# Performance work log

Measured on AMD Instinct MI355X. Metric: run time of the kernel, lower is better.

The kernel has to match this reference:

```python
import jax, jax.numpy as jnp
import numpy as np

B, C, S, D = 16, 32, 64, 512
DFF, E = 2048, 8


def setup_inputs() -> dict:
    key = jax.random.key(0)
    ks = jax.random.split(key, 16)
    std = 0.02
    return {
        'x': jax.random.normal(ks[0], (B, C, S, D), jnp.float32),
        'baseline': jax.random.normal(ks[1], (B, C, S, D), jnp.float32),
        'attnres': jax.random.normal(ks[2], (B, C, S, D), jnp.float32),
        'shared_w1': jax.random.normal(ks[3], (DFF, D), jnp.float32) * std,
        'shared_b1': jnp.zeros((DFF,), jnp.float32),
        'shared_w2': jax.random.normal(ks[4], (D, DFF), jnp.float32) * std,
        'shared_b2': jnp.zeros((D,), jnp.float32),
        'spa_router_w': jax.random.normal(ks[5], (E, 3 * D), jnp.float32) * std,
        'spa_router_b': jnp.zeros((E,), jnp.float32),
        'spe_router_w': jax.random.normal(ks[6], (E, 3 * D), jnp.float32) * std,
        'spe_router_b': jnp.zeros((E,), jnp.float32),
        'spa_w1': jax.random.normal(ks[7], (E, DFF, D), jnp.float32) * std,
        'spa_b1': jnp.zeros((E, DFF), jnp.float32),
        'spa_w2': jax.random.normal(ks[8], (E, D, DFF), jnp.float32) * std,
        'spa_b2': jnp.zeros((E, D), jnp.float32),
        'spe_w1': jax.random.normal(ks[9], (E, DFF, D), jnp.float32) * std,
        'spe_b1': jnp.zeros((E, DFF), jnp.float32),
        'spe_w2': jax.random.normal(ks[10], (E, D, DFF), jnp.float32) * std,
        'spe_b2': jnp.zeros((E, D), jnp.float32),
    }


def _route(feat, rw, rb):
    # feat [B, 3D] -> top-1 expert index [B] and its softmax gate weight [B]
    logits = feat @ rw.T + rb            # [B, E]
    p = jax.nn.softmax(logits, axis=-1)
    idx = jnp.argmax(logits, axis=-1)    # [B]
    w = jnp.take_along_axis(p, idx[:, None], axis=-1)[:, 0]
    return idx, w


def _specialist(xf, idx, w1, b1, w2, b2):
    # xf [B, T, D]; per-sample gather of expert weights then batched FFN
    W1, B1 = w1[idx], b1[idx]            # [B, DFF, D], [B, DFF]
    W2, B2 = w2[idx], b2[idx]            # [B, D, DFF], [B, D]
    h = jax.nn.gelu(jnp.einsum('btd,bfd->btf', xf, W1) + B1[:, None, :])
    return jnp.einsum('btf,bdf->btd', h, W2) + B2[:, None, :]


def reference(x, baseline, attnres, shared_w1, shared_b1, shared_w2, shared_b2,
              spa_router_w, spa_router_b, spe_router_w, spe_router_b,
              spa_w1, spa_b1, spa_w2, spa_b2, spe_w1, spe_b1, spe_w2, spe_b2):
    b, d = x.shape[0], x.shape[-1]
    xf = x.reshape(b, -1, d)  # [B, T, D]
    # sample-level AttnRes router features: [B, 3*d_model]
    feat = jnp.concatenate([
        baseline.mean(axis=(1, 2)),
        attnres.mean(axis=(1, 2)),
        (attnres - baseline).mean(axis=(1, 2)),
    ], axis=-1)
    spa_idx, spa_w = _route(feat, spa_router_w, spa_router_b)
    spe_idx, spe_w = _route(feat, spe_router_w, spe_router_b)
    # shared dense FFN (dropout=0 eval)
    shared = jax.nn.gelu(xf @ shared_w1.T + shared_b1) @ shared_w2.T + shared_b2
    spa_out = _specialist(xf, spa_idx, spa_w1, spa_b1, spa_w2, spa_b2)
    spe_out = _specialist(xf, spe_idx, spe_w1, spe_b1, spe_w2, spe_b2)
    y = shared + spa_w[:, None, None] * spa_out + spe_w[:, None, None] * spe_out
    return y.reshape(x.shape)
```

## Files before the change

kernel.cpp:

```cpp
#include <hip/hip_runtime.h>
#include <cstdint>
#include <cstddef>

#define DEV __device__ __forceinline__

typedef unsigned short u16;
typedef _Float16 f16x8 __attribute__((ext_vector_type(8)));
typedef float f32x4 __attribute__((ext_vector_type(4)));

static constexpr int NB  = 16;
static constexpr int T   = 2048;
static constexpr int D   = 512;
static constexpr int DFF = 2048;
static constexpr int NE  = 8;
static constexpr int FEAT = 3 * D;

#define MFMA16 __builtin_amdgcn_mfma_f32_16x16x32_f16

DEV u16 f2h(float f) {
  _Float16 h = (_Float16)f;
  union { _Float16 h; u16 u; } cv; cv.h = h; return cv.u;
}

DEV float gelu_fast(float x) {
  const float t = x * x;
  const float p = x * fmaf(t, -0.07135481627f, -1.59576912161f);
  return __fdividef(x, 1.0f + __expf(p));
}


__global__ void k_part(const float* __restrict__ base, const float* __restrict__ attn,
                       float* __restrict__ part) {
  const int b = blockIdx.x >> 4, ch = blockIdx.x & 15;
  const int d = threadIdx.x;
  const size_t o = ((size_t)b * T + (size_t)ch * 128) * D + d;
  const float* pb = base + o;
  const float* pa = attn + o;
  float sb = 0.f, sa = 0.f;
  for (int r = 0; r < 128; ++r) { sb += pb[(size_t)r * D]; sa += pa[(size_t)r * D]; }
  part[(b * 16 + ch) * D + d] = sb;
  part[NB * 16 * D + (b * 16 + ch) * D + d] = sa;
}

__global__ void k_feat(const float* __restrict__ part, float* __restrict__ feat) {
  const int b = blockIdx.x, d = threadIdx.x;
  float sb = 0.f, sa = 0.f;
  for (int ch = 0; ch < 16; ++ch) {
    sb += part[(b * 16 + ch) * D + d];
    sa += part[NB * 16 * D + (b * 16 + ch) * D + d];
  }
  sb *= (1.0f / 2048.0f); sa *= (1.0f / 2048.0f);
  feat[b * FEAT + d] = sb;
  feat[b * FEAT + D + d] = sa;
  feat[b * FEAT + 2 * D + d] = sa - sb;
}

__global__ void k_zero(int* __restrict__ used) {
  used[threadIdx.x] = 0;
}

__global__ void k_route(const float* __restrict__ feat,
                        const float* __restrict__ rw0, const float* __restrict__ rb0,
                        const float* __restrict__ rw1, const float* __restrict__ rb1,
                        int* __restrict__ idx, float* __restrict__ gate,
                        int* __restrict__ used) {
  const int r = blockIdx.x >> 4, b = blockIdx.x & 15;
  const float* rw = (r == 0) ? rw0 : rw1;
  const float* rb = (r == 0) ? rb0 : rb1;
  const int l = threadIdx.x;
  float p[8];
#pragma unroll
  for (int e = 0; e < 8; ++e) p[e] = 0.f;
  const float* f = feat + b * FEAT;
  for (int k = l; k < FEAT; k += 64) {
    const float fv = f[k];
#pragma unroll
    for (int e = 0; e < 8; ++e) p[e] += fv * rw[e * FEAT + k];
  }
#pragma unroll
  for (int off = 32; off >= 1; off >>= 1) {
#pragma unroll
    for (int e = 0; e < 8; ++e) p[e] += __shfl_xor(p[e], off);
  }
  if (l == 0) {
    float best = -1e30f; int bi = 0;
    float lg[8];
#pragma unroll
    for (int e = 0; e < 8; ++e) {
      lg[e] = p[e] + rb[e];
      if (lg[e] > best) { best = lg[e]; bi = e; }
    }
    float s = 0.f;
#pragma unroll
    for (int e = 0; e < 8; ++e) s += expf(lg[e] - best);
    idx[r * 16 + b] = bi;
    gate[r * 16 + b] = 1.0f / s;
    atomicOr(&used[r * 8 + bi], 1);
  }
}

__global__ void k_btot(const float* __restrict__ b2s, const float* __restrict__ b2a,
                       const float* __restrict__ b2e, const int* __restrict__ idx,
                       const float* __restrict__ gate, float* __restrict__ btot) {
  const int b = blockIdx.x, d = threadIdx.x;
  const int ia = idx[b], ie = idx[16 + b];
  const float ga = gate[b], ge = gate[16 + b];
  btot[b * D + d] = b2s[d] + ga * b2a[ia * D + d] + ge * b2e[ie * D + d];
}

__global__ void k_cast(const float* __restrict__ s, u16* __restrict__ d, long n) {
  const long i = ((long)blockIdx.x * blockDim.x + threadIdx.x) * 4;
  if (i >= n) return;
  const float4 v = *(const float4*)(s + i);
  const unsigned int lo = (unsigned int)f2h(v.x) | ((unsigned int)f2h(v.y) << 16);
  const unsigned int hi = (unsigned int)f2h(v.z) | ((unsigned int)f2h(v.w) << 16);
  *(uint2*)(d + i) = make_uint2(lo, hi);
}

__global__ void k_cast_gated(const float* __restrict__ s, u16* __restrict__ d,
                             const int* __restrict__ used) {
  const int e = blockIdx.x >> 10;
  if (!used[e]) return;
  const long i = (long)e * (DFF * D) + ((long)(blockIdx.x & 1023) * 256 + threadIdx.x) * 4;
  const float4 v = *(const float4*)(s + i);
  const unsigned int lo = (unsigned int)f2h(v.x) | ((unsigned int)f2h(v.y) << 16);
  const unsigned int hi = (unsigned int)f2h(v.z) | ((unsigned int)f2h(v.w) << 16);
  *(uint2*)(d + i) = make_uint2(lo, hi);
}


DEV void ld_lds16(const void* g, void* l) {
  __builtin_amdgcn_global_load_lds((const __attribute__((address_space(1))) void*)g,
                                   (__attribute__((address_space(3))) void*)l, 16, 0, 0);
}

#define BAR __builtin_amdgcn_s_barrier()
#define LGKM0 do { asm volatile("s_waitcnt lgkmcnt(0)" ::: "memory"); \
                   __builtin_amdgcn_sched_barrier(0); } while (0)
#define VMW2 asm volatile("s_waitcnt vmcnt(2)" ::: "memory")
#define VMW0 asm volatile("s_waitcnt vmcnt(0)" ::: "memory")

#define STG_A(tt, h, sb) do { const long ko_ = (long)(tt) * 64;                          \
    ld_lds16(((h) ? gA10 : gA00) + ko_, (char*)As + (sb) * 32768 + (h) * 16384 + dR0);   \
    ld_lds16(((h) ? gA11 : gA01) + ko_, (char*)As + (sb) * 32768 + (h) * 16384 + dR1); } while (0)
#define STG_B(tt, h, sb) do { const long ko_ = (long)(tt) * 64;                          \
    ld_lds16(((h) ? gB10 : gB00) + ko_, (char*)Bs + (sb) * 32768 + (h) * 16384 + dR0);   \
    ld_lds16(((h) ? gB11 : gB01) + ko_, (char*)Bs + (sb) * 32768 + (h) * 16384 + dR1); } while (0)

#define RD_A(dst, mb, sb) do {                                                           \
    _Pragma("unroll") for (int m_ = 0; m_ < 4; ++m_)                                     \
      _Pragma("unroll") for (int k_ = 0; k_ < 2; ++k_)                                   \
        dst[m_][k_] = *(const f16x8*)((const char*)As + (sb) * 32768 + avb[k_] +         \
                                      ((mb) + m_) * 2048); } while (0)
#define RD_B(dst, nb, sb) do {                                                           \
    _Pragma("unroll") for (int n_ = 0; n_ < 2; ++n_)                                     \
      _Pragma("unroll") for (int k_ = 0; k_ < 2; ++k_)                                   \
        dst[n_][k_] = *(const f16x8*)((const char*)Bs + (sb) * 32768 + bvb[k_] +         \
                                      ((nb) + n_) * 2048); } while (0)

#define QUAD(av, bv, mb, nb) do { __builtin_amdgcn_s_setprio(1);                         \
    _Pragma("unroll") for (int m_ = 0; m_ < 4; ++m_)                                     \
      _Pragma("unroll") for (int n_ = 0; n_ < 2; ++n_) {                                 \
        acc[(mb)+m_][(nb)+n_] = MFMA16(av[m_][0], bv[n_][0], acc[(mb)+m_][(nb)+n_],0,0,0); \
        acc[(mb)+m_][(nb)+n_] = MFMA16(av[m_][1], bv[n_][1], acc[(mb)+m_][(nb)+n_],0,0,0); \
      }                                                                                  \
    __builtin_amdgcn_s_setprio(0); } while (0)

#define TILE(tt, sb, STGN, STGA0, VMN) do {                                              \
                                                             \
    RD_A(avLO, 0, sb); RD_B(bvA, 0, sb);                                                 \
    if (STGN) { STG_A((tt)+1, 1, (sb)^1); STG_B((tt)+1, 0, (sb)^1); STG_B((tt)+1, 1, (sb)^1); } \
    BAR; LGKM0; QUAD(avLO, bvA, 0, 0); BAR;                                              \
                                                             \
    RD_B(bvB, 2, sb);                                                                    \
    BAR; LGKM0; QUAD(avLO, bvB, 0, 2); BAR;                                              \
                                                             \
    RD_A(avHI, 4, sb);                                                                   \
    BAR; LGKM0; QUAD(avHI, bvB, 4, 2); BAR;                                              \
                                                             \
    RD_B(bvA, 0, sb);                                                                    \
    if (STGA0) STG_A((tt)+2, 0, sb);                                                     \
    BAR; LGKM0; QUAD(avHI, bvA, 4, 0);                                                   \
    if ((VMN) == 2) VMW2; else if ((VMN) == 0) VMW0;                                     \
    BAR;                                                                                 \
  } while (0)

template <int NT>
DEV void gemm_8p(const u16* __restrict__ A, int lda, const u16* __restrict__ B, int ldb,
                 u16* As, u16* Bs, f32x4 (&acc)[8][4]) {
  static_assert(NT >= 6 && (NT % 2) == 0, "NT must be even and >= 6");
  const int tid = threadIdx.x;
  const int lane = tid & 63, wid = tid >> 6;
  const int wr = wid >> 2, wc = wid & 3;

  const int srow = lane >> 3;
  const int scol = (lane & 7) ^ srow;
  const int rj0 = wid * 16 + srow;
  const int rj1 = rj0 + 8;
  const u16* gA00 = A + (size_t)(  0 + rj0) * lda + scol * 8;
  const u16* gA01 = A + (size_t)(  0 + rj1) * lda + scol * 8;
  const u16* gA10 = A + (size_t)(128 + rj0) * lda + scol * 8;
  const u16* gA11 = A + (size_t)(128 + rj1) * lda + scol * 8;
  const u16* gB00 = B + (size_t)(  0 + rj0) * ldb + scol * 8;
  const u16* gB01 = B + (size_t)(  0 + rj1) * ldb + scol * 8;
  const u16* gB10 = B + (size_t)(128 + rj0) * ldb + scol * 8;
  const u16* gB11 = B + (size_t)(128 + rj1) * ldb + scol * 8;
  const int dR0 = (wid * 16) * 128;
  const int dR1 = dR0 + 1024;

  const int aR = wr * 128 + (lane & 15);
  const int bR = wc * 64 + (lane & 15);
  const int sH = lane >> 4;
  int avb[2], bvb[2];
#pragma unroll
  for (int k_ = 0; k_ < 2; ++k_) {
    const int s_ = (k_ * 4 + sH);
    avb[k_] = aR * 128 + ((s_ ^ (lane & 7)) * 16);
    bvb[k_] = bR * 128 + ((s_ ^ (lane & 7)) * 16);
  }

  f16x8 avLO[4][2], avHI[4][2], bvA[2][2], bvB[2][2];

  STG_A(0, 0, 0); STG_A(0, 1, 0); STG_B(0, 0, 0); STG_B(0, 1, 0);
  STG_A(1, 0, 1);
  VMW2; BAR;

  for (int tp = 0; tp < (NT - 2) / 2; ++tp) {
    TILE(2 * tp,     0, true, true, 2);
    TILE(2 * tp + 1, 1, true, true, 2);
  }
  TILE(NT - 2, 0, true,  false, 0);
  TILE(NT - 1, 1, false, false, -1);
}

template <int BANK>
__global__ __launch_bounds__(512) void k_ffn1(
    const u16* __restrict__ xh, const u16* __restrict__ w1, const float* __restrict__ b1,
    const int* __restrict__ idx, const float* __restrict__ gate, u16* __restrict__ h) {
  __shared__ alignas(16) u16 As[2 * 16384];
  __shared__ alignas(16) u16 Bs[2 * 16384];
  int wg = blockIdx.x;
  const int q = (int)gridDim.x >> 3;
  wg = (wg & 7) * q + (wg >> 3);
  const int b  = wg >> 6;
  const int mt = (wg >> 3) & 7;
  const int nt = wg & 7;

  const int e   = (BANK == 0) ? 0 : idx[(BANK - 1) * 16 + b];
  const float g = (BANK == 0) ? 1.0f : gate[(BANK - 1) * 16 + b];
  const u16* Ab = xh + ((size_t)b * T + (size_t)mt * 256) * D;
  const u16* Bb = w1 + (size_t)e * DFF * D + (size_t)nt * 256 * D;
  const float* bb = b1 + (size_t)e * DFF;

  f32x4 acc[8][4];
#pragma unroll
  for (int m = 0; m < 8; ++m)
#pragma unroll
    for (int n = 0; n < 4; ++n)
#pragma unroll
      for (int r = 0; r < 4; ++r) acc[m][n][r] = 0.f;

  gemm_8p<8>(Ab, D, Bb, D, As, Bs, acc);

  const int lane = threadIdx.x & 63, wid = threadIdx.x >> 6;
  const int wr = wid >> 2, wc = wid & 3;
  const int rr = (lane >> 4) << 2, cc = lane & 15;
  const int mrow = mt * 256 + wr * 128;
  const int ncol = nt * 256 + wc * 64;
  u16* hb = h + (size_t)b * T * DFF;
  float bias[4];
#pragma unroll
  for (int n = 0; n < 4; ++n) bias[n] = bb[ncol + n * 16 + cc];
#pragma unroll
  for (int m = 0; m < 8; ++m) {
    const int row = mrow + m * 16 + rr;
#pragma unroll
    for (int n = 0; n < 4; ++n) {
      const int col = ncol + n * 16 + cc;
      const f32x4 a = acc[m][n];
#pragma unroll
      for (int r = 0; r < 4; ++r) {
        const float v = gelu_fast(a[r] + bias[n]) * g;
        hb[(size_t)(row + r) * DFF + col] = f2h(v);
      }
    }
  }
}

template <int BANK>
__global__ __launch_bounds__(512) void k_ffn2(
    const u16* __restrict__ h, const u16* __restrict__ w2, const float* __restrict__ btot,
    const int* __restrict__ idx, float* __restrict__ out) {
  __shared__ alignas(16) u16 As[2 * 16384];
  __shared__ alignas(16) u16 Bs[2 * 16384];
  int wg = blockIdx.x;
  const int q = (int)gridDim.x >> 3;
  wg = (wg & 7) * q + (wg >> 3);
  const int b  = wg >> 4;
  const int mt = (wg >> 1) & 7;
  const int nt = wg & 1;

  const int e = (BANK == 0) ? 0 : idx[(BANK - 1) * 16 + b];
  const u16* Ab = h + ((size_t)b * T + (size_t)mt * 256) * DFF;
  const u16* Bb = w2 + (size_t)e * D * DFF + (size_t)nt * 256 * DFF;

  f32x4 acc[8][4];
#pragma unroll
  for (int m = 0; m < 8; ++m)
#pragma unroll
    for (int n = 0; n < 4; ++n)
#pragma unroll
      for (int r = 0; r < 4; ++r) acc[m][n][r] = 0.f;

  gemm_8p<32>(Ab, DFF, Bb, DFF, As, Bs, acc);

  const int lane = threadIdx.x & 63, wid = threadIdx.x >> 6;
  const int wr = wid >> 2, wc = wid & 3;
  const int rr = (lane >> 4) << 2, cc = lane & 15;
  const int mrow = mt * 256 + wr * 128;
  const int ncol = nt * 256 + wc * 64;
  float* ob = out + (size_t)b * T * D;
  const float* bt = btot + b * D;
  float btv[4];
#pragma unroll
  for (int n = 0; n < 4; ++n) btv[n] = bt[ncol + n * 16 + cc];
#pragma unroll
  for (int m = 0; m < 8; ++m) {
    const int row = mrow + m * 16 + rr;
#pragma unroll
    for (int n = 0; n < 4; ++n) {
      const int col = ncol + n * 16 + cc;
      const f32x4 a = acc[m][n];
#pragma unroll
      for (int r = 0; r < 4; ++r) {
        const size_t oi = (size_t)(row + r) * D + col;
        if (BANK == 0) ob[oi] = a[r] + btv[n];
        else           ob[oi] += a[r];
      }
    }
  }
}


extern "C" void kernel_launch(void* const* d_in, const int* in_sizes, int n_in,
                              void* d_out, int out_size, void* d_ws, size_t ws_size,
                              hipStream_t stream) {
  (void)in_sizes; (void)n_in; (void)out_size; (void)ws_size;
  const float* x    = (const float*)d_in[0];
  const float* base = (const float*)d_in[1];
  const float* attn = (const float*)d_in[2];
  const float* sw1  = (const float*)d_in[3];
  const float* sb1  = (const float*)d_in[4];
  const float* sw2  = (const float*)d_in[5];
  const float* sb2  = (const float*)d_in[6];
  const float* arw  = (const float*)d_in[7];
  const float* arb  = (const float*)d_in[8];
  const float* erw  = (const float*)d_in[9];
  const float* erb  = (const float*)d_in[10];
  const float* aw1  = (const float*)d_in[11];
  const float* ab1  = (const float*)d_in[12];
  const float* aw2  = (const float*)d_in[13];
  const float* ab2  = (const float*)d_in[14];
  const float* ew1  = (const float*)d_in[15];
  const float* eb1  = (const float*)d_in[16];
  const float* ew2  = (const float*)d_in[17];
  const float* eb2  = (const float*)d_in[18];
  float* out = (float*)d_out;

  char* w = (char*)d_ws;
  u16* xh   = (u16*)w;  w += (size_t)NB * T * D * 2;
  u16* hbuf = (u16*)w;  w += (size_t)NB * T * DFF * 2;
  u16* w1s  = (u16*)w;  w += (size_t)DFF * D * 2;
  u16* w2s  = (u16*)w;  w += (size_t)D * DFF * 2;
  u16* w1a  = (u16*)w;  w += (size_t)NE * DFF * D * 2;
  u16* w2a  = (u16*)w;  w += (size_t)NE * D * DFF * 2;
  u16* w1e  = (u16*)w;  w += (size_t)NE * DFF * D * 2;
  u16* w2e  = (u16*)w;  w += (size_t)NE * D * DFF * 2;
  float* part = (float*)w; w += (size_t)2 * NB * 16 * D * 4;
  float* feat = (float*)w; w += (size_t)NB * FEAT * 4;
  int*   idx  = (int*)w;   w += 32 * 4;
  float* gate = (float*)w; w += 32 * 4;
  float* btot = (float*)w; w += (size_t)NB * D * 4;
  int*   used = (int*)w;   w += 16 * 4;

  k_zero<<<dim3(1), dim3(16), 0, stream>>>(used);
  k_part<<<dim3(256), dim3(512), 0, stream>>>(base, attn, part);
  k_feat<<<dim3(16), dim3(512), 0, stream>>>(part, feat);
  k_route<<<dim3(32), dim3(64), 0, stream>>>(feat, arw, arb, erw, erb, idx, gate, used);
  k_btot<<<dim3(16), dim3(512), 0, stream>>>(sb2, ab2, eb2, idx, gate, btot);

  {
    long n;
    n = (long)NB * T * D;  k_cast<<<(unsigned)(n / 1024), 256, 0, stream>>>(x,   xh,  n);
    n = (long)DFF * D;     k_cast<<<(unsigned)(n / 1024), 256, 0, stream>>>(sw1, w1s, n);
    n = (long)D * DFF;     k_cast<<<(unsigned)(n / 1024), 256, 0, stream>>>(sw2, w2s, n);
    k_cast_gated<<<dim3(8192), 256, 0, stream>>>(aw1, w1a, used);
    k_cast_gated<<<dim3(8192), 256, 0, stream>>>(aw2, w2a, used);
    k_cast_gated<<<dim3(8192), 256, 0, stream>>>(ew1, w1e, used + 8);
    k_cast_gated<<<dim3(8192), 256, 0, stream>>>(ew2, w2e, used + 8);
  }

  const dim3 g1(1024), g2(256), blk(512);
  k_ffn1<0><<<g1, blk, 0, stream>>>(xh, w1s, sb1, idx, gate, hbuf);
  k_ffn2<0><<<g2, blk, 0, stream>>>(hbuf, w2s, btot, idx, out);
  k_ffn1<1><<<g1, blk, 0, stream>>>(xh, w1a, ab1, idx, gate, hbuf);
  k_ffn2<1><<<g2, blk, 0, stream>>>(hbuf, w2a, btot, idx, out);
  k_ffn1<2><<<g1, blk, 0, stream>>>(xh, w1e, eb1, idx, gate, hbuf);
  k_ffn2<2><<<g2, blk, 0, stream>>>(hbuf, w2e, btot, idx, out);
}
```

Before: 727.9 us.

## Stage GEMM epilogues through LDS for vectorized stores and reuse B fragment

Both FFN kernels now write their accumulator tiles into a per-wave LDS scratch region, then read them back in row-contiguous order and issue 16-byte global stores (and 16-byte read-modify-write for the accumulation banks). This replaces the earlier scattered 2-byte and 4-byte strided stores. Separately, the last quarter of the GEMM tile reuses the bvA B-fragment already in registers instead of re-reading it from LDS, which drops one LDS read and its wait. The epilogue reuses the As buffer as scratch, which relies on the main loop having finished with it.

```diff
diff --git a/kernel.cpp b/kernel.cpp
--- a/kernel.cpp
+++ b/kernel.cpp
@@ -167,20 +167,15 @@
     __builtin_amdgcn_s_setprio(0); } while (0)
 
 #define TILE(tt, sb, STGN, STGA0, VMN) do {                                              \
-                                                             \
     RD_A(avLO, 0, sb); RD_B(bvA, 0, sb);                                                 \
     if (STGN) { STG_A((tt)+1, 1, (sb)^1); STG_B((tt)+1, 0, (sb)^1); STG_B((tt)+1, 1, (sb)^1); } \
     BAR; LGKM0; QUAD(avLO, bvA, 0, 0); BAR;                                              \
-                                                             \
     RD_B(bvB, 2, sb);                                                                    \
     BAR; LGKM0; QUAD(avLO, bvB, 0, 2); BAR;                                              \
-                                                             \
     RD_A(avHI, 4, sb);                                                                   \
     BAR; LGKM0; QUAD(avHI, bvB, 4, 2); BAR;                                              \
-                                                             \
-    RD_B(bvA, 0, sb);                                                                    \
     if (STGA0) STG_A((tt)+2, 0, sb);                                                     \
-    BAR; LGKM0; QUAD(avHI, bvA, 4, 0);                                                   \
+    BAR; __builtin_amdgcn_sched_barrier(0); QUAD(avHI, bvA, 4, 0);                       \
     if ((VMN) == 2) VMW2; else if ((VMN) == 0) VMW0;                                     \
     BAR;                                                                                 \
   } while (0)
@@ -188,7 +183,7 @@
 template <int NT>
 DEV void gemm_8p(const u16* __restrict__ A, int lda, const u16* __restrict__ B, int ldb,
                  u16* As, u16* Bs, f32x4 (&acc)[8][4]) {
-  static_assert(NT >= 6 && (NT % 2) == 0, "NT must be even and >= 6");
+  static_assert(NT >= 8 && (NT % 2) == 0, "NT even, >= 8");
   const int tid = threadIdx.x;
   const int lane = tid & 63, wid = tid >> 6;
   const int wr = wid >> 2, wc = wid & 3;
@@ -268,22 +263,30 @@
   const int mrow = mt * 256 + wr * 128;
   const int ncol = nt * 256 + wc * 64;
   u16* hb = h + (size_t)b * T * DFF;
+  u16* wsl = (u16*)As + wid * (16 * 72);
+  const int rdrow = lane >> 2;
+  const int rdcb  = (lane & 3) * 2;
   float bias[4];
 #pragma unroll
   for (int n = 0; n < 4; ++n) bias[n] = bb[ncol + n * 16 + cc];
 #pragma unroll
   for (int m = 0; m < 8; ++m) {
-    const int row = mrow + m * 16 + rr;
 #pragma unroll
     for (int n = 0; n < 4; ++n) {
-      const int col = ncol + n * 16 + cc;
       const f32x4 a = acc[m][n];
 #pragma unroll
-      for (int r = 0; r < 4; ++r) {
-        const float v = gelu_fast(a[r] + bias[n]) * g;
-        hb[(size_t)(row + r) * DFF + col] = f2h(v);
-      }
+      for (int r = 0; r < 4; ++r)
+        wsl[(rr + r) * 72 + n * 16 + cc] = f2h(gelu_fast(a[r] + bias[n]) * g);
     }
+    asm volatile("s_waitcnt lgkmcnt(0)" ::: "memory");
+    __builtin_amdgcn_sched_barrier(0);
+    const uint4 v0 = *(const uint4*)(wsl + rdrow * 72 + rdcb * 8);
+    const uint4 v1 = *(const uint4*)(wsl + rdrow * 72 + rdcb * 8 + 8);
+    u16* dst = hb + (size_t)(mrow + m * 16 + rdrow) * DFF + ncol + rdcb * 8;
+    *(uint4*)dst = v0;
+    *(uint4*)(dst + 8) = v1;
+    asm volatile("s_waitcnt lgkmcnt(0)" ::: "memory");
+    __builtin_amdgcn_sched_barrier(0);
   }
 }
 
@@ -320,24 +323,33 @@
   const int mrow = mt * 256 + wr * 128;
   const int ncol = nt * 256 + wc * 64;
   float* ob = out + (size_t)b * T * D;
-  const float* bt = btot + b * D;
+  float* wsl = (float*)(void*)As + wid * (16 * 68);
   float btv[4];
 #pragma unroll
-  for (int n = 0; n < 4; ++n) btv[n] = bt[ncol + n * 16 + cc];
+  for (int n = 0; n < 4; ++n)
+    btv[n] = (BANK == 0) ? btot[b * D + ncol + n * 16 + cc] : 0.f;
 #pragma unroll
   for (int m = 0; m < 8; ++m) {
-    const int row = mrow + m * 16 + rr;
 #pragma unroll
     for (int n = 0; n < 4; ++n) {
-      const int col = ncol + n * 16 + cc;
       const f32x4 a = acc[m][n];
 #pragma unroll
-      for (int r = 0; r < 4; ++r) {
-        const size_t oi = (size_t)(row + r) * D + col;
-        if (BANK == 0) ob[oi] = a[r] + btv[n];
-        else           ob[oi] += a[r];
-      }
+      for (int r = 0; r < 4; ++r)
+        wsl[(rr + r) * 68 + n * 16 + cc] = a[r] + btv[n];
     }
+    asm volatile("s_waitcnt lgkmcnt(0)" ::: "memory");
+    __builtin_amdgcn_sched_barrier(0);
+#pragma unroll
+    for (int j = 0; j < 4; ++j) {
+      const int row = j * 4 + (lane >> 4);
+      const int colb = lane & 15;
+      f32x4 v = *(const f32x4*)(wsl + row * 68 + colb * 4);
+      float* dst = ob + (size_t)(mrow + m * 16 + row) * D + ncol + colb * 4;
+      if (BANK != 0) { const f32x4 o = *(const f32x4*)dst; v += o; }
+      *(f32x4*)dst = v;
+    }
+    asm volatile("s_waitcnt lgkmcnt(0)" ::: "memory");
+    __builtin_amdgcn_sched_barrier(0);
   }
 }
 
```

New measurement: 719.1 us. About the same (-1.2%).
